# Kernel optimization log

Measured on AMD Instinct MI355X. Metric: run time of the kernel, lower is better.

## Reference

```python
import jax, jax.numpy as jnp
import numpy as np

N_OCC, N_SKILL, N_EDGE = 20000, 50000, 600000
D_IN, HID, OUT = 256, 128, 64


def _sage(x_src, x_dst, src, dst, Wl, bl, Wr, n_dst):
    """PyG SAGEConv((in,in),out): mean-aggregate neighbor msgs, lin_l + lin_r(x_dst)."""
    msg = x_src[src]                                        # [E, h] gather
    agg = jax.ops.segment_sum(msg, dst, num_segments=n_dst) # [n_dst, h]
    cnt = jax.ops.segment_sum(jnp.ones((src.shape[0],), x_src.dtype), dst,
                              num_segments=n_dst)
    mean = agg / jnp.maximum(cnt, 1.0)[:, None]
    return mean @ Wl + bl + x_dst @ Wr


def setup_inputs() -> dict:
    key = jax.random.key(0)
    ks = jax.random.split(key, 24)
    f32 = jnp.float32

    def lin(k, fi, fo):
        return jax.random.normal(k, (fi, fo), f32) / np.sqrt(fi)

    inp = {
        "x_occ": jax.random.normal(ks[0], (N_OCC, D_IN), f32),
        "x_skill": jax.random.normal(ks[1], (N_SKILL, D_IN), f32),
        "edge_occ": jax.random.randint(ks[2], (N_EDGE,), 0, N_OCC, jnp.int32),
        "edge_skill": jax.random.randint(ks[3], (N_EDGE,), 0, N_SKILL, jnp.int32),
        # input projections (nn.Linear with bias)
        "pW_occ": lin(ks[4], D_IN, HID), "pb_occ": jnp.zeros((HID,), f32),
        "pW_skill": lin(ks[5], D_IN, HID), "pb_skill": jnp.zeros((HID,), f32),
        # conv1: occ->skill and skill->occ SAGEConvs (lin_l has bias, lin_r none)
        "c1_os_Wl": lin(ks[6], HID, HID), "c1_os_bl": jnp.zeros((HID,), f32),
        "c1_os_Wr": lin(ks[7], HID, HID),
        "c1_so_Wl": lin(ks[8], HID, HID), "c1_so_bl": jnp.zeros((HID,), f32),
        "c1_so_Wr": lin(ks[9], HID, HID),
        # conv2
        "c2_os_Wl": lin(ks[10], HID, OUT), "c2_os_bl": jnp.zeros((OUT,), f32),
        "c2_os_Wr": lin(ks[11], HID, OUT),
        "c2_so_Wl": lin(ks[12], HID, OUT), "c2_so_bl": jnp.zeros((OUT,), f32),
        "c2_so_Wr": lin(ks[13], HID, OUT),
    }
    return inp


def reference(x_occ, x_skill, edge_occ, edge_skill,
              pW_occ, pb_occ, pW_skill, pb_skill,
              c1_os_Wl, c1_os_bl, c1_os_Wr, c1_so_Wl, c1_so_bl, c1_so_Wr,
              c2_os_Wl, c2_os_bl, c2_os_Wr, c2_so_Wl, c2_so_bl, c2_so_Wr):
    n_occ, n_skill = x_occ.shape[0], x_skill.shape[0]
    # input proj + relu
    h_occ = jax.nn.relu(x_occ @ pW_occ + pb_occ)
    h_skill = jax.nn.relu(x_skill @ pW_skill + pb_skill)
    # conv1 (HeteroConv aggr='sum'; each node type receives exactly one conv)
    s1 = _sage(h_occ, h_skill, edge_occ, edge_skill, c1_os_Wl, c1_os_bl, c1_os_Wr, n_skill)
    o1 = _sage(h_skill, h_occ, edge_skill, edge_occ, c1_so_Wl, c1_so_bl, c1_so_Wr, n_occ)
    o1, s1 = jax.nn.relu(o1), jax.nn.relu(s1)
    # conv2
    s2 = _sage(o1, s1, edge_occ, edge_skill, c2_os_Wl, c2_os_bl, c2_os_Wr, n_skill)
    o2 = _sage(s1, o1, edge_skill, edge_occ, c2_so_Wl, c2_so_bl, c2_so_Wr, n_occ)
    return o2, s2
```

## Files before the change

kernel.cpp:

```cpp
#include <hip/hip_runtime.h>

#define N_OCC   20000
#define N_SKILL 50000
#define N_EDGE  600000
#define D_IN    256
#define HID     128
#define OUT_F   64

typedef short bf16x8 __attribute__((ext_vector_type(8)));
typedef float f32x4  __attribute__((ext_vector_type(4)));

__device__ __forceinline__ float bf2f(unsigned short u){
  return __uint_as_float(((unsigned)u) << 16);
}
__device__ __forceinline__ unsigned f2bf_bits(float f){
  unsigned i = __float_as_uint(f);
  return (i + 0x7fffu + ((i >> 16) & 1u)) >> 16;
}
__device__ __forceinline__ unsigned f2bf_bits_u(unsigned i){
  return (i + 0x7fffu + ((i >> 16) & 1u)) >> 16;
}
__device__ __forceinline__ unsigned short f2bf(float f){ return (unsigned short)f2bf_bits(f); }

__global__ void k_detect(const unsigned short* __restrict__ x, int* __restrict__ flag){
  int lane = threadIdx.x & 63;
  int cnt = 0;
  for (int i = lane; i < 1024; i += 64){
    unsigned e = ((unsigned)x[i] >> 7) & 0xFFu;
    if (e >= 0xE0u) cnt++;
  }
  #pragma unroll
  for (int s = 1; s < 64; s <<= 1) cnt += __shfl_xor(cnt, s, 64);
  if (lane == 0) *flag = (cnt >= 8) ? 1 : 0;
}

#define NT_CONV 16
struct ConvTable {
  const void*     src[NT_CONV];
  unsigned short* dst[NT_CONV];
  int             n[NT_CONV];
  int             blk_off[NT_CONV + 1];
};

__global__ void k_convert(ConvTable t, const int* __restrict__ flag){
  int isf32 = *flag;
  int b = blockIdx.x;
  int ti = 0;
  while (ti < NT_CONV - 1 && b >= t.blk_off[ti + 1]) ti++;
  int lb = b - t.blk_off[ti];
  int i = (lb * 256 + (int)threadIdx.x) * 8;
  if (i >= t.n[ti]) return;
  unsigned short* dst = t.dst[ti];
  if (isf32){
    const float* s = (const float*)t.src[ti];
    uint4 lo = *(const uint4*)(s + i);
    uint4 hi = *(const uint4*)(s + i + 4);
    uint4 o;
    o.x = f2bf_bits_u(lo.x) | (f2bf_bits_u(lo.y) << 16);
    o.y = f2bf_bits_u(lo.z) | (f2bf_bits_u(lo.w) << 16);
    o.z = f2bf_bits_u(hi.x) | (f2bf_bits_u(hi.y) << 16);
    o.w = f2bf_bits_u(hi.z) | (f2bf_bits_u(hi.w) << 16);
    *(uint4*)(dst + i) = o;
  } else {
    *(uint4*)(dst + i) = *(const uint4*)((const unsigned short*)t.src[ti] + i);
  }
}

__global__ void k_transpose_all(
    const unsigned short* pWo, unsigned short* tWo,
    const unsigned short* pWs, unsigned short* tWs,
    const unsigned short* w2,  unsigned short* t2,
    const unsigned short* w3,  unsigned short* t3,
    const unsigned short* w4,  unsigned short* t4,
    const unsigned short* w5,  unsigned short* t5,
    const unsigned short* w6,  unsigned short* t6,
    const unsigned short* w7,  unsigned short* t7,
    const unsigned short* w8,  unsigned short* t8,
    const unsigned short* w9,  unsigned short* t9)
{
  int idx = blockIdx.x * blockDim.x + threadIdx.x;
  const unsigned short* in; unsigned short* out; int K, N, base;
  if      (idx <  32768){ in=pWo; out=tWo; K=256; N=128; base=0; }
  else if (idx <  65536){ in=pWs; out=tWs; K=256; N=128; base=32768; }
  else if (idx <  81920){ in=w2;  out=t2;  K=128; N=128; base=65536; }
  else if (idx <  98304){ in=w3;  out=t3;  K=128; N=128; base=81920; }
  else if (idx < 114688){ in=w4;  out=t4;  K=128; N=128; base=98304; }
  else if (idx < 131072){ in=w5;  out=t5;  K=128; N=128; base=114688; }
  else if (idx < 139264){ in=w6;  out=t6;  K=128; N=64;  base=131072; }
  else if (idx < 147456){ in=w7;  out=t7;  K=128; N=64;  base=139264; }
  else if (idx < 155648){ in=w8;  out=t8;  K=128; N=64;  base=147456; }
  else if (idx < 163840){ in=w9;  out=t9;  K=128; N=64;  base=155648; }
  else return;
  int li = idx - base;
  int k = li / N, n = li - k * N;
  out[n * K + k] = in[li];
}

#define EPB      4096
#define BIN_BLKS ((N_EDGE + EPB - 1) / EPB)
#define SH_S 9
#define SH_O 8
#define NB_S ((N_SKILL + (1 << SH_S) - 1) >> SH_S)
#define NB_O ((N_OCC   + (1 << SH_O) - 1) >> SH_O)

__launch_bounds__(256)
__global__ void k_bincount(const int* __restrict__ eo, const int* __restrict__ es,
                           int* __restrict__ bkcnt_s, int* __restrict__ bkcnt_o)
{
  int b = blockIdx.x;
  int side = (b >= BIN_BLKS) ? 1 : 0;
  int lb = side ? b - BIN_BLKS : b;
  const int* dste = side ? eo : es;
  int* bkcnt = side ? bkcnt_o : bkcnt_s;
  const int NB = side ? NB_O : NB_S;
  const int SH = side ? SH_O : SH_S;
  __shared__ int cntL[NB_S];
  for (int i = threadIdx.x; i < NB; i += 256) cntL[i] = 0;
  __syncthreads();
  int e0 = lb * EPB, e1 = min(e0 + EPB, N_EDGE);
  for (int e = e0 + threadIdx.x; e < e1; e += 256)
    atomicAdd(&cntL[dste[e] >> SH], 1);
  __syncthreads();
  for (int i = threadIdx.x; i < NB; i += 256)
    if (cntL[i]) atomicAdd(&bkcnt[i], cntL[i]);
}

__global__ void k_bscan(const int* __restrict__ bkcnt_s, const int* __restrict__ bkcnt_o,
                        int* __restrict__ boff_s, int* __restrict__ boff_o,
                        int* __restrict__ off_s, int* __restrict__ off_o)
{
  __shared__ int sc[128];
  int t = threadIdx.x;
  int v = (t < NB_S) ? bkcnt_s[t] : 0;
  sc[t] = v;
  __syncthreads();
  for (int d = 1; d < 128; d <<= 1){
    int u = (t >= d) ? sc[t - d] : 0;
    __syncthreads();
    sc[t] += u;
    __syncthreads();
  }
  if (t < NB_S) boff_s[t] = sc[t] - v;
  if (t == 0){ boff_s[NB_S] = N_EDGE; off_s[N_SKILL] = N_EDGE; }
  __syncthreads();
  int v2 = (t < NB_O) ? bkcnt_o[t] : 0;
  sc[t] = v2;
  __syncthreads();
  for (int d = 1; d < 128; d <<= 1){
    int u = (t >= d) ? sc[t - d] : 0;
    __syncthreads();
    sc[t] += u;
    __syncthreads();
  }
  if (t < NB_O) boff_o[t] = sc[t] - v2;
  if (t == 0){ boff_o[NB_O] = N_EDGE; off_o[N_OCC] = N_EDGE; }
}

__launch_bounds__(256)
__global__ void k_bin(const int* __restrict__ eo, const int* __restrict__ es,
                      const int* __restrict__ boff_s, const int* __restrict__ boff_o,
                      int* __restrict__ bcur_s, int* __restrict__ bcur_o,
                      unsigned* __restrict__ pair_s, unsigned* __restrict__ pair_o)
{
  int b = blockIdx.x;
  int side = (b >= BIN_BLKS) ? 1 : 0;
  int lb = side ? b - BIN_BLKS : b;
  const int* dste = side ? eo : es;
  const int* srce = side ? es : eo;
  const int* boff = side ? boff_o : boff_s;
  int* bcur       = side ? bcur_o : bcur_s;
  unsigned* pairs = side ? pair_o : pair_s;
  const int NB = side ? NB_O : NB_S;
  const int SH = side ? SH_O : SH_S;

  __shared__ int cntL[NB_S], gbaseL[NB_S], lbaseL[NB_S], runL[NB_S];
  __shared__ int sc[128];
  __shared__ unsigned stage[EPB];
  __shared__ int gpos[EPB];

  int e0 = lb * EPB;
  int e1 = min(e0 + EPB, N_EDGE);

  for (int i = threadIdx.x; i < NB; i += 256){ cntL[i] = 0; runL[i] = 0; }
  __syncthreads();
  for (int e = e0 + threadIdx.x; e < e1; e += 256)
    atomicAdd(&cntL[dste[e] >> SH], 1);
  __syncthreads();
  if (threadIdx.x < 128) sc[threadIdx.x] = (threadIdx.x < NB) ? cntL[threadIdx.x] : 0;
  __syncthreads();
  for (int d = 1; d < 128; d <<= 1){
    int v = 0;
    if (threadIdx.x < 128 && threadIdx.x >= d) v = sc[threadIdx.x - d];
    __syncthreads();
    if (threadIdx.x < 128) sc[threadIdx.x] += v;
    __syncthreads();
  }
  if (threadIdx.x < NB){
    int c = cntL[threadIdx.x];
    lbaseL[threadIdx.x] = sc[threadIdx.x] - c;
    gbaseL[threadIdx.x] = boff[threadIdx.x] + atomicAdd(&bcur[threadIdx.x], c);
  }
  __syncthreads();
  for (int e = e0 + threadIdx.x; e < e1; e += 256){
    int d = dste[e], s = srce[e];
    int bk = d >> SH;
    int r = atomicAdd(&runL[bk], 1);
    int lp = lbaseL[bk] + r;
    stage[lp] = ((unsigned)(d & ((1 << SH) - 1)) << 16) | (unsigned)s;
    gpos[lp] = gbaseL[bk] + r;
  }
  __syncthreads();
  int tot = e1 - e0;
  for (int i = threadIdx.x; i < tot; i += 256)
    pairs[gpos[i]] = stage[i];
}

__launch_bounds__(256)
__global__ void k_build(const unsigned* __restrict__ pair_s, const unsigned* __restrict__ pair_o,
                        const int* __restrict__ boff_s, const int* __restrict__ boff_o,
                        int* __restrict__ off_s, int* __restrict__ off_o,
                        int* __restrict__ csr_s, int* __restrict__ csr_o)
{
  int b = blockIdx.x;
  int side = (b >= NB_S) ? 1 : 0;
  int lb = side ? b - NB_S : b;
  const unsigned* pairs = side ? pair_o : pair_s;
  const int* boff = side ? boff_o : boff_s;
  int* off = side ? off_o : off_s;
  int* csr = side ? csr_o : csr_s;
  int SH = side ? SH_O : SH_S;
  int nd_tot = side ? N_OCC : N_SKILL;
  int d0 = lb << SH;
  int d1 = min(d0 + (1 << SH), nd_tot);
  int nd = d1 - d0;
  int p0 = boff[lb], p1 = boff[lb + 1];

  __shared__ int cntL[1 << SH_S];
  __shared__ int offL[1 << SH_S];
  __shared__ int ws[4];
  int t = threadIdx.x;
  cntL[t] = 0; cntL[t + 256] = 0;
  __syncthreads();
  for (int i = p0 + t; i < p1; i += 256)
    atomicAdd(&cntL[pairs[i] >> 16], 1);
  __syncthreads();
  int a0 = cntL[2 * t], a1 = cntL[2 * t + 1];
  int s = a0 + a1;
  int lane = t & 63, wv = t >> 6;
  int x = s;
  #pragma unroll
  for (int d = 1; d < 64; d <<= 1){ int u = __shfl_up(x, d, 64); if (lane >= d) x += u; }
  if (lane == 63) ws[wv] = x;
  __syncthreads();
  int woff = 0;
  for (int w = 0; w < wv; ++w) woff += ws[w];
  int excl = woff + x - s;
  offL[2 * t] = excl;
  offL[2 * t + 1] = excl + a0;
  __syncthreads();
  for (int i = t; i < nd; i += 256) off[d0 + i] = p0 + offL[i];
  cntL[t] = 0; cntL[t + 256] = 0;
  __syncthreads();
  for (int i = p0 + t; i < p1; i += 256){
    unsigned pr = pairs[i];
    int d = (int)(pr >> 16);
    int p = p0 + offL[d] + atomicAdd(&cntL[d], 1);
    csr[p] = (int)(pr & 0xFFFFu);
  }
}

__launch_bounds__(256)
__global__ void k_seg_mean2(const unsigned short* __restrict__ feat0,
                            const int* __restrict__ off0, const int* __restrict__ csr0,
                            unsigned short* __restrict__ out0, int n0, int nb0,
                            const unsigned short* __restrict__ feat1,
                            const int* __restrict__ off1, const int* __restrict__ csr1,
                            unsigned short* __restrict__ out1, int n1)
{
  int b = blockIdx.x;
  int side = (b >= nb0) ? 1 : 0;
  const unsigned short* feat = side ? feat1 : feat0;
  const int* off = side ? off1 : off0;
  const int* csr = side ? csr1 : csr0;
  unsigned short* out = side ? out1 : out0;
  int n_dst = side ? n1 : n0;
  int gw = (side ? b - nb0 : b) * 4 + (int)(threadIdx.x >> 6);
  if (gw >= n_dst) return;
  int lane = threadIdx.x & 63;
  int r = lane >> 4;
  int c = lane & 15;
  int beg = off[gw], end = off[gw + 1];
  float acc[8];
  #pragma unroll
  for (int j = 0; j < 8; ++j) acc[j] = 0.0f;
  for (int e = beg + r; e < end; e += 4){
    int s = csr[e];
    uint4 v = *(const uint4*)(feat + ((size_t)s << 7) + (c << 3));
    acc[0] += __uint_as_float(v.x << 16); acc[1] += __uint_as_float(v.x & 0xffff0000u);
    acc[2] += __uint_as_float(v.y << 16); acc[3] += __uint_as_float(v.y & 0xffff0000u);
    acc[4] += __uint_as_float(v.z << 16); acc[5] += __uint_as_float(v.z & 0xffff0000u);
    acc[6] += __uint_as_float(v.w << 16); acc[7] += __uint_as_float(v.w & 0xffff0000u);
  }
  #pragma unroll
  for (int j = 0; j < 8; ++j){
    acc[j] += __shfl_xor(acc[j], 16, 64);
    acc[j] += __shfl_xor(acc[j], 32, 64);
  }
  if (r == 0){
    int cnt = end - beg;
    float inv = 1.0f / (float)(cnt > 0 ? cnt : 1);
    uint4 o;
    o.x = f2bf_bits(acc[0] * inv) | (f2bf_bits(acc[1] * inv) << 16);
    o.y = f2bf_bits(acc[2] * inv) | (f2bf_bits(acc[3] * inv) << 16);
    o.z = f2bf_bits(acc[4] * inv) | (f2bf_bits(acc[5] * inv) << 16);
    o.w = f2bf_bits(acc[6] * inv) | (f2bf_bits(acc[7] * inv) << 16);
    *(uint4*)(out + ((size_t)gw << 7) + (c << 3)) = o;
  }
}

__launch_bounds__(256)
__global__ void k_seg_out2(const unsigned short* __restrict__ Pg0, const unsigned short* __restrict__ Ps0,
                           const int* __restrict__ off0, const int* __restrict__ csr0,
                           const unsigned short* __restrict__ bias0, size_t o_off0, int n0, int nb0,
                           const unsigned short* __restrict__ Pg1, const unsigned short* __restrict__ Ps1,
                           const int* __restrict__ off1, const int* __restrict__ csr1,
                           const unsigned short* __restrict__ bias1, size_t o_off1, int n1,
                           void* __restrict__ out, const int* __restrict__ wire_flag)
{
  int b = blockIdx.x;
  int side = (b >= nb0) ? 1 : 0;
  const unsigned short* Pg = side ? Pg1 : Pg0;
  const unsigned short* Ps = side ? Ps1 : Ps0;
  const int* off = side ? off1 : off0;
  const int* csr = side ? csr1 : csr0;
  const unsigned short* bias = side ? bias1 : bias0;
  size_t o_off = side ? o_off1 : o_off0;
  int n_dst = side ? n1 : n0;
  int gw = (side ? b - nb0 : b) * 4 + (int)(threadIdx.x >> 6);
  if (gw >= n_dst) return;
  int lane = threadIdx.x & 63;
  int r = lane >> 3;
  int c = lane & 7;
  int beg = off[gw], end = off[gw + 1];
  float acc[8];
  #pragma unroll
  for (int j = 0; j < 8; ++j) acc[j] = 0.0f;
  for (int e = beg + r; e < end; e += 8){
    int s = csr[e];
    uint4 v = *(const uint4*)(Pg + ((size_t)s << 7) + (c << 3));
    acc[0] += __uint_as_float(v.x << 16); acc[1] += __uint_as_float(v.x & 0xffff0000u);
    acc[2] += __uint_as_float(v.y << 16); acc[3] += __uint_as_float(v.y & 0xffff0000u);
    acc[4] += __uint_as_float(v.z << 16); acc[5] += __uint_as_float(v.z & 0xffff0000u);
    acc[6] += __uint_as_float(v.w << 16); acc[7] += __uint_as_float(v.w & 0xffff0000u);
  }
  #pragma unroll
  for (int j = 0; j < 8; ++j){
    acc[j] += __shfl_xor(acc[j], 8, 64);
    acc[j] += __shfl_xor(acc[j], 16, 64);
    acc[j] += __shfl_xor(acc[j], 32, 64);
  }
  if (r == 0){
    int cnt = end - beg;
    float inv = 1.0f / (float)(cnt > 0 ? cnt : 1);
    uint4 sv = *(const uint4*)(Ps + ((size_t)gw << 7) + 64 + (c << 3));
    uint4 bv = *(const uint4*)(bias + (c << 3));
    float o0 = acc[0] * inv + __uint_as_float(sv.x << 16)         + __uint_as_float(bv.x << 16);
    float o1 = acc[1] * inv + __uint_as_float(sv.x & 0xffff0000u) + __uint_as_float(bv.x & 0xffff0000u);
    float o2 = acc[2] * inv + __uint_as_float(sv.y << 16)         + __uint_as_float(bv.y << 16);
    float o3 = acc[3] * inv + __uint_as_float(sv.y & 0xffff0000u) + __uint_as_float(bv.y & 0xffff0000u);
    float o4 = acc[4] * inv + __uint_as_float(sv.z << 16)         + __uint_as_float(bv.z << 16);
    float o5 = acc[5] * inv + __uint_as_float(sv.z & 0xffff0000u) + __uint_as_float(bv.z & 0xffff0000u);
    float o6 = acc[6] * inv + __uint_as_float(sv.w << 16)         + __uint_as_float(bv.w << 16);
    float o7 = acc[7] * inv + __uint_as_float(sv.w & 0xffff0000u) + __uint_as_float(bv.w & 0xffff0000u);
    size_t eoff = o_off + (size_t)gw * 64 + (c << 3);
    if (*wire_flag){
      float* op = (float*)out + eoff;
      uint4 w0, w1;
      w0.x = __float_as_uint(o0); w0.y = __float_as_uint(o1);
      w0.z = __float_as_uint(o2); w0.w = __float_as_uint(o3);
      w1.x = __float_as_uint(o4); w1.y = __float_as_uint(o5);
      w1.z = __float_as_uint(o6); w1.w = __float_as_uint(o7);
      *(uint4*)op = w0;
      *(uint4*)(op + 4) = w1;
    } else {
      unsigned short* op = (unsigned short*)out + eoff;
      uint4 w;
      w.x = f2bf_bits(o0) | (f2bf_bits(o1) << 16);
      w.y = f2bf_bits(o2) | (f2bf_bits(o3) << 16);
      w.z = f2bf_bits(o4) | (f2bf_bits(o5) << 16);
      w.w = f2bf_bits(o6) | (f2bf_bits(o7) << 16);
      *(uint4*)op = w;
    }
  }
}

template<int K1, int HASA2, int AW>
__launch_bounds__(256)
__global__ void k_gemm2(const unsigned short* __restrict__ A1_0, const unsigned short* __restrict__ A1_1,
                        const unsigned short* __restrict__ W1T_0, const unsigned short* __restrict__ W1T_1,
                        const unsigned short* __restrict__ A2_0, const unsigned short* __restrict__ A2_1,
                        const unsigned short* __restrict__ W2T_0, const unsigned short* __restrict__ W2T_1,
                        const unsigned short* __restrict__ bias_0, const unsigned short* __restrict__ bias_1,
                        unsigned short* __restrict__ C_0, unsigned short* __restrict__ C_1,
                        int M0, int M1, int nb0, int do_relu,
                        const int* __restrict__ wire_flag)
{
  constexpr int NK = K1 / 32;
  int b = blockIdx.x;
  int side = (b >= nb0) ? 1 : 0;
  const unsigned short* A1  = side ? A1_1  : A1_0;
  const unsigned short* W1T = side ? W1T_1 : W1T_0;
  const unsigned short* A2  = side ? A2_1  : A2_0;
  const unsigned short* W2T = side ? W2T_1 : W2T_0;
  const unsigned short* bias= side ? bias_1: bias_0;
  unsigned short* C = side ? C_1 : C_0;
  int M = side ? M1 : M0;
  int lb = side ? b - nb0 : b;

  const int lane = threadIdx.x & 63;
  const int wv   = threadIdx.x >> 6;
  const int q    = lane >> 4;
  const int mr   = lane & 15;
  const int m0   = lb * 64 + wv * 16;
  const int koff = q * 8;
  const int row  = m0 + mr;
  const int arow = (row < M) ? row : (M - 1);

  f32x4 acc[8];
  #pragma unroll
  for (int nt = 0; nt < 8; ++nt)
    #pragma unroll
    for (int j = 0; j < 4; ++j) acc[nt][j] = 0.0f;

  bf16x8 afr1[NK];
  bf16x8 afr2[HASA2 ? NK : 1];

  if (AW && *wire_flag){
    const float* ap = (const float*)A1 + (size_t)arow * K1 + koff;
    #pragma unroll
    for (int k = 0; k < NK; ++k){
      uint4 lo = *(const uint4*)(ap + k * 32);
      uint4 hi = *(const uint4*)(ap + k * 32 + 4);
      union { bf16x8 v; uint4 u; } cv;
      cv.u.x = f2bf_bits_u(lo.x) | (f2bf_bits_u(lo.y) << 16);
      cv.u.y = f2bf_bits_u(lo.z) | (f2bf_bits_u(lo.w) << 16);
      cv.u.z = f2bf_bits_u(hi.x) | (f2bf_bits_u(hi.y) << 16);
      cv.u.w = f2bf_bits_u(hi.z) | (f2bf_bits_u(hi.w) << 16);
      afr1[k] = cv.v;
    }
  } else {
    const unsigned short* ap = A1 + (size_t)arow * K1 + koff;
    #pragma unroll
    for (int k = 0; k < NK; ++k)
      afr1[k] = *(const bf16x8*)(ap + k * 32);
  }
  if (HASA2){
    const unsigned short* ap2 = A2 + (size_t)arow * K1 + koff;
    #pragma unroll
    for (int k = 0; k < NK; ++k)
      afr2[k] = *(const bf16x8*)(ap2 + k * 32);
  }

  #pragma unroll
  for (int k = 0; k < NK; ++k){
    const int k0 = k * 32;
    #pragma unroll
    for (int nt = 0; nt < 8; ++nt){
      bf16x8 b1 = *(const bf16x8*)(W1T + (size_t)(nt * 16 + mr) * K1 + k0 + koff);
      acc[nt] = __builtin_amdgcn_mfma_f32_16x16x32_bf16(afr1[k], b1, acc[nt], 0, 0, 0);
    }
    if (HASA2){
      #pragma unroll
      for (int nt = 0; nt < 8; ++nt){
        bf16x8 b2 = *(const bf16x8*)(W2T + (size_t)(nt * 16 + mr) * K1 + k0 + koff);
        acc[nt] = __builtin_amdgcn_mfma_f32_16x16x32_bf16(afr2[k], b2, acc[nt], 0, 0, 0);
      }
    }
  }

  #pragma unroll
  for (int nt = 0; nt < 8; ++nt){
    int col = nt * 16 + mr;
    float bv = bf2f(bias[col]);
    #pragma unroll
    for (int r4 = 0; r4 < 4; ++r4){
      int orow = m0 + q * 4 + r4;
      if (orow < M){
        float v = acc[nt][r4] + bv;
        if (do_relu) v = fmaxf(v, 0.0f);
        C[(size_t)orow * 128 + col] = f2bf(v);
      }
    }
  }
}

extern "C" void kernel_launch(void* const* d_in, const int* in_sizes, int n_in,
                              void* d_out, int out_size, void* d_ws, size_t ws_size,
                              hipStream_t stream)
{
  const void* raw[20];
  for (int i = 0; i < 20; ++i) raw[i] = d_in[i];
  const int* edge_occ   = (const int*)d_in[2];
  const int* edge_skill = (const int*)d_in[3];

  char* ws = (char*)d_ws;
  size_t off = 0;
  auto alloc = [&](size_t bytes) -> char* {
    char* p = ws + off;
    off = (off + bytes + 255) & ~(size_t)255;
    return p;
  };

  int* wire_flag = (int*)alloc(4);

  static const int cn[NT_CONV] = {
    D_IN * HID, HID, D_IN * HID, HID,
    HID * HID, HID, HID * HID,
    HID * HID, HID, HID * HID,
    HID * OUT_F, OUT_F, HID * OUT_F,
    HID * OUT_F, OUT_F, HID * OUT_F
  };
  static const int raw_idx[NT_CONV] = {4,5,6,7, 8,9,10, 11,12,13, 14,15,16, 17,18,19};
  unsigned short* can[NT_CONV];
  for (int i = 0; i < NT_CONV; ++i) can[i] = (unsigned short*)alloc((size_t)cn[i] * 2);

  ConvTable ct;
  ct.blk_off[0] = 0;
  for (int i = 0; i < NT_CONV; ++i){
    ct.src[i] = raw[raw_idx[i]];
    ct.dst[i] = can[i];
    ct.n[i]   = cn[i];
    ct.blk_off[i + 1] = ct.blk_off[i] + (cn[i] + 2047) / 2048;
  }
  const int conv_blocks = ct.blk_off[NT_CONV];

  const unsigned short* c_pWo = can[0],  *c_pbo = can[1];
  const unsigned short* c_pWs = can[2],  *c_pbs = can[3];
  const unsigned short* c1osWl = can[4], *c1osbl = can[5], *c1osWr = can[6];
  const unsigned short* c1soWl = can[7], *c1sobl = can[8], *c1soWr = can[9];
  const unsigned short* c2osWl = can[10], *c2osbl = can[11], *c2osWr = can[12];
  const unsigned short* c2soWl = can[13], *c2sobl = can[14], *c2soWr = can[15];

  unsigned short* wt_pocc   = (unsigned short*)alloc(32768 * 2);
  unsigned short* wt_pskill = (unsigned short*)alloc(32768 * 2);
  unsigned short* wt_c1osWl = (unsigned short*)alloc(16384 * 2);
  unsigned short* wt_c1osWr = (unsigned short*)alloc(16384 * 2);
  unsigned short* wt_c1soWl = (unsigned short*)alloc(16384 * 2);
  unsigned short* wt_c1soWr = (unsigned short*)alloc(16384 * 2);
  unsigned short* comb_occ  = (unsigned short*)alloc(16384 * 2);
  unsigned short* comb_skl  = (unsigned short*)alloc(16384 * 2);

  size_t zero_bytes = (size_t)(2 * (NB_S + NB_O)) * 4 + 256;
  char* zero_base = alloc(zero_bytes);
  int* bkcnt_s = (int*)zero_base;
  int* bkcnt_o = bkcnt_s + NB_S;
  int* bcur_s  = bkcnt_o + NB_O;
  int* bcur_o  = bcur_s + NB_S;
  unsigned short* zbias = (unsigned short*)(bcur_o + NB_O);

  int* boff_s = (int*)alloc((NB_S + 1) * 4);
  int* boff_o = (int*)alloc((NB_O + 1) * 4);
  int* off_s = (int*)alloc((N_SKILL + 1) * 4);
  int* off_o = (int*)alloc((N_OCC + 1) * 4);
  int* csr_s = (int*)alloc((size_t)N_EDGE * 4);
  int* csr_o = (int*)alloc((size_t)N_EDGE * 4);
  unsigned* pair_s = (unsigned*)alloc((size_t)N_EDGE * 4);
  unsigned* pair_o = (unsigned*)alloc((size_t)N_EDGE * 4);

  unsigned short* h_occ   = (unsigned short*)alloc((size_t)N_OCC * HID * 2);
  unsigned short* h_skill = (unsigned short*)alloc((size_t)N_SKILL * HID * 2);
  unsigned short* mean_s  = (unsigned short*)alloc((size_t)N_SKILL * HID * 2);
  unsigned short* mean_o  = (unsigned short*)alloc((size_t)N_OCC * HID * 2);
  unsigned short* s1      = (unsigned short*)alloc((size_t)N_SKILL * HID * 2);
  unsigned short* o1      = (unsigned short*)alloc((size_t)N_OCC * HID * 2);
  unsigned short* P_occ   = (unsigned short*)alloc((size_t)N_OCC * HID * 2);
  unsigned short* P_skl   = (unsigned short*)alloc((size_t)N_SKILL * HID * 2);

  const int GB_OCC = (N_OCC + 63) / 64;
  const int GB_SKL = (N_SKILL + 63) / 64;
  const int SM_SKL = (N_SKILL + 3) / 4;
  const int SM_OCC = (N_OCC + 3) / 4;

  hipMemsetAsync(zero_base, 0, zero_bytes, stream);

  k_detect<<<1, 64, 0, stream>>>((const unsigned short*)raw[0], wire_flag);
  k_convert<<<conv_blocks, 256, 0, stream>>>(ct, wire_flag);

  k_transpose_all<<<640, 256, 0, stream>>>(
      c_pWo, wt_pocc, c_pWs, wt_pskill,
      c1osWl, wt_c1osWl, c1osWr, wt_c1osWr,
      c1soWl, wt_c1soWl, c1soWr, wt_c1soWr,
      c2osWl, comb_occ,
      c2osWr, comb_skl + 64 * 128,
      c2soWl, comb_skl,
      c2soWr, comb_occ + 64 * 128);

  k_bincount<<<2 * BIN_BLKS, 256, 0, stream>>>(edge_occ, edge_skill, bkcnt_s, bkcnt_o);
  k_bscan<<<1, 128, 0, stream>>>(bkcnt_s, bkcnt_o, boff_s, boff_o, off_s, off_o);
  k_bin<<<2 * BIN_BLKS, 256, 0, stream>>>(edge_occ, edge_skill, boff_s, boff_o,
                                          bcur_s, bcur_o, pair_s, pair_o);
  k_build<<<NB_S + NB_O, 256, 0, stream>>>(pair_s, pair_o, boff_s, boff_o,
                                           off_s, off_o, csr_s, csr_o);

  k_gemm2<256, 0, 1><<<GB_OCC + GB_SKL, 256, 0, stream>>>(
      (const unsigned short*)raw[0], (const unsigned short*)raw[1],
      wt_pocc, wt_pskill, nullptr, nullptr, nullptr, nullptr,
      c_pbo, c_pbs, h_occ, h_skill, N_OCC, N_SKILL, GB_OCC, 1, wire_flag);

  k_seg_mean2<<<SM_SKL + SM_OCC, 256, 0, stream>>>(
      h_occ, off_s, csr_s, mean_s, N_SKILL, SM_SKL,
      h_skill, off_o, csr_o, mean_o, N_OCC);

  k_gemm2<128, 1, 0><<<GB_SKL + GB_OCC, 256, 0, stream>>>(
      mean_s, mean_o, wt_c1osWl, wt_c1soWl,
      h_skill, h_occ, wt_c1osWr, wt_c1soWr,
      c1osbl, c1sobl, s1, o1, N_SKILL, N_OCC, GB_SKL, 1, wire_flag);

  k_gemm2<128, 0, 0><<<GB_OCC + GB_SKL, 256, 0, stream>>>(
      o1, s1, comb_occ, comb_skl, nullptr, nullptr, nullptr, nullptr,
      zbias, zbias, P_occ, P_skl, N_OCC, N_SKILL, GB_OCC, 0, wire_flag);

  k_seg_out2<<<SM_SKL + SM_OCC, 256, 0, stream>>>(
      P_occ, P_skl, off_s, csr_s, c2osbl, (size_t)N_OCC * OUT_F, N_SKILL, SM_SKL,
      P_skl, P_occ, off_o, csr_o, c2sobl, 0, N_OCC,
      d_out, wire_flag);
}
```

Measured before the change: 393.3 us.

## Split GEMM output columns across waves with register-resident weight fragments

Restructures the dense GEMM kernel so each block handles 16 rows and each of its four waves computes a 32-column slice. Each wave preloads its weight fragments into registers once instead of reloading all 128 columns' weights per k-step, and the grid grows fourfold. The cost is that all four waves re-read the same A rows, and each block does less work, so launch and scheduling overhead rise. Grid sizes now use exact division, which relies on the node counts being multiples of 16.

```diff
diff --git a/kernel.cpp b/kernel.cpp
--- a/kernel.cpp
+++ b/kernel.cpp
@@ -396,7 +396,7 @@
 
 template<int K1, int HASA2, int AW>
 __launch_bounds__(256)
-__global__ void k_gemm2(const unsigned short* __restrict__ A1_0, const unsigned short* __restrict__ A1_1,
+__global__ void k_gemm3(const unsigned short* __restrict__ A1_0, const unsigned short* __restrict__ A1_1,
                         const unsigned short* __restrict__ W1T_0, const unsigned short* __restrict__ W1T_1,
                         const unsigned short* __restrict__ A2_0, const unsigned short* __restrict__ A2_1,
                         const unsigned short* __restrict__ W2T_0, const unsigned short* __restrict__ W2T_1,
@@ -421,20 +421,31 @@
   const int wv   = threadIdx.x >> 6;
   const int q    = lane >> 4;
   const int mr   = lane & 15;
-  const int m0   = lb * 64 + wv * 16;
+  const int m0   = lb * 16;
   const int koff = q * 8;
   const int row  = m0 + mr;
   const int arow = (row < M) ? row : (M - 1);
 
-  f32x4 acc[8];
-  #pragma unroll
-  for (int nt = 0; nt < 8; ++nt)
-    #pragma unroll
-    for (int j = 0; j < 4; ++j) acc[nt][j] = 0.0f;
-
-  bf16x8 afr1[NK];
-  bf16x8 afr2[HASA2 ? NK : 1];
-
+  bf16x8 b1[2][NK];
+  #pragma unroll
+  for (int nt = 0; nt < 2; ++nt){
+    const unsigned short* bp = W1T + (size_t)(wv * 32 + nt * 16 + mr) * K1 + koff;
+    #pragma unroll
+    for (int k = 0; k < NK; ++k)
+      b1[nt][k] = *(const bf16x8*)(bp + k * 32);
+  }
+  bf16x8 b2[2][HASA2 ? NK : 1];
+  if (HASA2){
+    #pragma unroll
+    for (int nt = 0; nt < 2; ++nt){
+      const unsigned short* bp = W2T + (size_t)(wv * 32 + nt * 16 + mr) * K1 + koff;
+      #pragma unroll
+      for (int k = 0; k < NK; ++k)
+        b2[nt][k] = *(const bf16x8*)(bp + k * 32);
+    }
+  }
+
+  bf16x8 a1[NK];
   if (AW && *wire_flag){
     const float* ap = (const float*)A1 + (size_t)arow * K1 + koff;
     #pragma unroll
@@ -446,41 +457,41 @@
       cv.u.y = f2bf_bits_u(lo.z) | (f2bf_bits_u(lo.w) << 16);
       cv.u.z = f2bf_bits_u(hi.x) | (f2bf_bits_u(hi.y) << 16);
       cv.u.w = f2bf_bits_u(hi.z) | (f2bf_bits_u(hi.w) << 16);
-      afr1[k] = cv.v;
+      a1[k] = cv.v;
     }
   } else {
     const unsigned short* ap = A1 + (size_t)arow * K1 + koff;
     #pragma unroll
     for (int k = 0; k < NK; ++k)
-      afr1[k] = *(const bf16x8*)(ap + k * 32);
-  }
+      a1[k] = *(const bf16x8*)(ap + k * 32);
+  }
+  bf16x8 a2[HASA2 ? NK : 1];
   if (HASA2){
     const unsigned short* ap2 = A2 + (size_t)arow * K1 + koff;
     #pragma unroll
     for (int k = 0; k < NK; ++k)
-      afr2[k] = *(const bf16x8*)(ap2 + k * 32);
-  }
+      a2[k] = *(const bf16x8*)(ap2 + k * 32);
+  }
+
+  f32x4 acc[2];
+  #pragma unroll
+  for (int nt = 0; nt < 2; ++nt)
+    #pragma unroll
+    for (int j = 0; j < 4; ++j) acc[nt][j] = 0.0f;
 
   #pragma unroll
   for (int k = 0; k < NK; ++k){
-    const int k0 = k * 32;
-    #pragma unroll
-    for (int nt = 0; nt < 8; ++nt){
-      bf16x8 b1 = *(const bf16x8*)(W1T + (size_t)(nt * 16 + mr) * K1 + k0 + koff);
-      acc[nt] = __builtin_amdgcn_mfma_f32_16x16x32_bf16(afr1[k], b1, acc[nt], 0, 0, 0);
+    #pragma unroll
+    for (int nt = 0; nt < 2; ++nt){
+      acc[nt] = __builtin_amdgcn_mfma_f32_16x16x32_bf16(a1[k], b1[nt][k], acc[nt], 0, 0, 0);
+      if (HASA2)
+        acc[nt] = __builtin_amdgcn_mfma_f32_16x16x32_bf16(a2[k], b2[nt][k], acc[nt], 0, 0, 0);
     }
-    if (HASA2){
-      #pragma unroll
-      for (int nt = 0; nt < 8; ++nt){
-        bf16x8 b2 = *(const bf16x8*)(W2T + (size_t)(nt * 16 + mr) * K1 + k0 + koff);
-        acc[nt] = __builtin_amdgcn_mfma_f32_16x16x32_bf16(afr2[k], b2, acc[nt], 0, 0, 0);
-      }
-    }
-  }
-
-  #pragma unroll
-  for (int nt = 0; nt < 8; ++nt){
-    int col = nt * 16 + mr;
+  }
+
+  #pragma unroll
+  for (int nt = 0; nt < 2; ++nt){
+    int col = wv * 32 + nt * 16 + mr;
     float bv = bf2f(bias[col]);
     #pragma unroll
     for (int r4 = 0; r4 < 4; ++r4){
@@ -576,8 +587,8 @@
   unsigned short* P_occ   = (unsigned short*)alloc((size_t)N_OCC * HID * 2);
   unsigned short* P_skl   = (unsigned short*)alloc((size_t)N_SKILL * HID * 2);
 
-  const int GB_OCC = (N_OCC + 63) / 64;
-  const int GB_SKL = (N_SKILL + 63) / 64;
+  const int GB_OCC = N_OCC / 16;
+  const int GB_SKL = N_SKILL / 16;
   const int SM_SKL = (N_SKILL + 3) / 4;
   const int SM_OCC = (N_OCC + 3) / 4;
 
@@ -602,7 +613,7 @@
   k_build<<<NB_S + NB_O, 256, 0, stream>>>(pair_s, pair_o, boff_s, boff_o,
                                            off_s, off_o, csr_s, csr_o);
 
-  k_gemm2<256, 0, 1><<<GB_OCC + GB_SKL, 256, 0, stream>>>(
+  k_gemm3<256, 0, 1><<<GB_OCC + GB_SKL, 256, 0, stream>>>(
       (const unsigned short*)raw[0], (const unsigned short*)raw[1],
       wt_pocc, wt_pskill, nullptr, nullptr, nullptr, nullptr,
       c_pbo, c_pbs, h_occ, h_skill, N_OCC, N_SKILL, GB_OCC, 1, wire_flag);
@@ -611,12 +622,12 @@
       h_occ, off_s, csr_s, mean_s, N_SKILL, SM_SKL,
       h_skill, off_o, csr_o, mean_o, N_OCC);
 
-  k_gemm2<128, 1, 0><<<GB_SKL + GB_OCC, 256, 0, stream>>>(
+  k_gemm3<128, 1, 0><<<GB_SKL + GB_OCC, 256, 0, stream>>>(
       mean_s, mean_o, wt_c1osWl, wt_c1soWl,
       h_skill, h_occ, wt_c1osWr, wt_c1soWr,
       c1osbl, c1sobl, s1, o1, N_SKILL, N_OCC, GB_SKL, 1, wire_flag);
 
-  k_gemm2<128, 0, 0><<<GB_OCC + GB_SKL, 256, 0, stream>>>(
+  k_gemm3<128, 0, 0><<<GB_OCC + GB_SKL, 256, 0, stream>>>(
       o1, s1, comb_occ, comb_skl, nullptr, nullptr, nullptr, nullptr,
       zbias, zbias, P_occ, P_skl, N_OCC, N_SKILL, GB_OCC, 0, wire_flag);
 
```

After: 408.0 us. 3.7% more time.
